# Optimization experiments

Hardware: AMD Instinct MI355X
Metric: run time of the kernel (lower is better)

## Reference

```python
import jax, jax.numpy as jnp
import numpy as np

N_HEAD = 12

def setup_inputs() -> dict:
    key = jax.random.key(0)
    k1, k2, k3, k4, k5 = jax.random.split(key, 5)
    B, T, C = 16, 1024, 768
    s = 0.02
    return {
        "x": jax.random.normal(k1, (B, T, C), dtype=jnp.float32),
        "W_attn": jax.random.normal(k2, (C, 3 * C), dtype=jnp.float32) * s,
        "b_attn": jax.random.normal(k3, (3 * C,), dtype=jnp.float32) * s,
        "W_proj": jax.random.normal(k4, (C, C), dtype=jnp.float32) * s,
        "b_proj": jax.random.normal(k5, (C,), dtype=jnp.float32) * s,
    }

def reference(x, W_attn, b_attn, W_proj, b_proj):
    B, T, C = x.shape
    H = N_HEAD
    d = C // H
    qkv = x @ W_attn + b_attn                      # [B,T,3C]
    q, k, v = jnp.split(qkv, 3, axis=-1)
    # [B,H,T,d]
    q = q.reshape(B, T, H, d).transpose(0, 2, 1, 3)
    k = k.reshape(B, T, H, d).transpose(0, 2, 1, 3)
    v = v.reshape(B, T, H, d).transpose(0, 2, 1, 3)
    scale = 1.0 / jnp.sqrt(jnp.array(d, dtype=x.dtype))
    att = jnp.einsum('bhqd,bhkd->bhqk', q, k) * scale   # [B,H,T,T]
    causal = jnp.tril(jnp.ones((T, T), dtype=bool))
    att = jnp.where(causal[None, None], att, -jnp.inf)
    att = jax.nn.softmax(att, axis=-1)
    # dropout is identity in eval mode (p=0 for deterministic reference)
    y = jnp.einsum('bhqk,bhkd->bhqd', att, v)            # [B,H,T,d]
    y = y.transpose(0, 2, 1, 3).reshape(B, T, C)
    return y @ W_proj + b_proj
```

## Files before the change

### kernel.cpp

```cpp
#include <hip/hip_runtime.h>
#include <cstddef>


typedef __bf16 bf16_t;
typedef __bf16 bf16x4 __attribute__((ext_vector_type(4)));
typedef __bf16 bf16x8 __attribute__((ext_vector_type(8)));
typedef float  f32x4  __attribute__((ext_vector_type(4)));

#define MFMA16(a,b,c) __builtin_amdgcn_mfma_f32_16x16x32_bf16((a),(b),(c),0,0,0)
#define GLOAD16(gp, lp) \
  __builtin_amdgcn_global_load_lds((const __attribute__((address_space(1))) unsigned int*)(gp), \
                                   (__attribute__((address_space(3))) unsigned int*)(lp), 16, 0, 0)

#define SWZ(row, c) (((row) * 64) + ((((c) ^ ((row) & 7)) * 8)))

#define QSCALE 0.1803368801111f

__global__ __launch_bounds__(256)
void xcast_kernel(const float* __restrict__ in, bf16_t* __restrict__ out)
{
    const size_t i = ((size_t)blockIdx.x * 256 + threadIdx.x) * 4;
    float4 f = *(const float4*)(in + i);
    bf16x4 o = {(bf16_t)f.x, (bf16_t)f.y, (bf16_t)f.z, (bf16_t)f.w};
    *(bf16x4*)(out + i) = o;
}

__global__ __launch_bounds__(256)
void tcast_kernel(const float* __restrict__ in, bf16_t* __restrict__ out, int R, int Cn)
{
    __shared__ bf16_t tile[32][33];
    const int tx = threadIdx.x & 31, ty = threadIdx.x >> 5;
    const int c0 = blockIdx.x * 32, r0 = blockIdx.y * 32;
#pragma unroll
    for (int i = 0; i < 4; ++i)
        tile[ty + i*8][tx] = (bf16_t)in[(size_t)(r0 + ty + i*8) * Cn + c0 + tx];
    __syncthreads();
#pragma unroll
    for (int i = 0; i < 4; ++i)
        out[(size_t)(c0 + ty + i*8) * R + r0 + tx] = tile[tx][ty + i*8];
}

__global__ __launch_bounds__(256)
void vtrans_kernel(const bf16_t* __restrict__ in, bf16_t* __restrict__ out)
{
    __shared__ bf16_t tile[32][33];
    const int tx = threadIdx.x & 31, ty = threadIdx.x >> 5;
    const int t0 = blockIdx.x * 32, c0 = blockIdx.y * 32;
    const size_t base = (size_t)blockIdx.z * 65536;
#pragma unroll
    for (int i = 0; i < 4; ++i)
        tile[ty + i*8][tx] = in[base + (size_t)(t0 + ty + i*8) * 64 + c0 + tx];
    __syncthreads();
#pragma unroll
    for (int i = 0; i < 4; ++i)
        out[base + (size_t)(c0 + ty + i*8) * 1024 + t0 + tx] = tile[tx][ty + i*8];
}

__global__ __launch_bounds__(256)
void qkv_gemm(const bf16_t* __restrict__ Xb, const bf16_t* __restrict__ WT,
              const float* __restrict__ bias,
              bf16_t* __restrict__ Qb, bf16_t* __restrict__ Kb, bf16_t* __restrict__ Vb)
{
    __shared__ bf16_t As[128 * 64];
    __shared__ bf16_t Bs[128 * 64];
    const int tid = threadIdx.x;
    const int w = tid >> 6, l = tid & 63;
    const int lm = l & 15, lq = l >> 4;
    const int wy = w >> 1, wx = w & 1;
    const int lr = l >> 3;
    const int lcs = ((l & 7) ^ lr) * 8;
    const int nt = blockIdx.x * 128, mt = blockIdx.y * 128;

    f32x4 acc[4][4];
    const f32x4 z4 = {0.f, 0.f, 0.f, 0.f};
#pragma unroll
    for (int i = 0; i < 4; ++i)
#pragma unroll
        for (int j = 0; j < 4; ++j) acc[i][j] = z4;

    for (int kt = 0; kt < 768; kt += 64) {
#pragma unroll
        for (int p = 0; p < 4; ++p) {
            const int row = w * 32 + p * 8;
            GLOAD16(Xb + (size_t)(mt + row + lr) * 768 + kt + lcs, &As[row * 64]);
            GLOAD16(WT + (size_t)(nt + row + lr) * 768 + kt + lcs, &Bs[row * 64]);
        }
        __syncthreads();
#pragma unroll
        for (int ks = 0; ks < 2; ++ks) {
            const int c = ks * 4 + lq;
            bf16x8 aw[4], bx[4];
#pragma unroll
            for (int i = 0; i < 4; ++i)
                aw[i] = *(const bf16x8*)(&Bs[SWZ(wx * 64 + i * 16 + lm, c)]);
#pragma unroll
            for (int j = 0; j < 4; ++j)
                bx[j] = *(const bf16x8*)(&As[SWZ(wy * 64 + j * 16 + lm, c)]);
#pragma unroll
            for (int i = 0; i < 4; ++i)
#pragma unroll
                for (int j = 0; j < 4; ++j)
                    acc[i][j] = MFMA16(aw[i], bx[j], acc[i][j]);
        }
        __syncthreads();
    }

    const int nb = nt + wx * 64;
    const int which = nb / 768;
    const int h = (nb % 768) >> 6;
    bf16_t* dst = (which == 0) ? Qb : ((which == 1) ? Kb : Vb);
    const float qs = (which == 0) ? QSCALE : 1.0f;
    const int b_ = mt >> 10;
    const int tbase = (mt & 1023) + wy * 64;
#pragma unroll
    for (int i = 0; i < 4; ++i) {
        const float4 bv = *(const float4*)(bias + nb + i * 16 + lq * 4);
        const int d0 = i * 16 + lq * 4;
#pragma unroll
        for (int j = 0; j < 4; ++j) {
            const int t = tbase + j * 16 + lm;
            f32x4 v = acc[i][j];
            bf16x4 o4 = {(bf16_t)((v[0] + bv.x) * qs), (bf16_t)((v[1] + bv.y) * qs),
                         (bf16_t)((v[2] + bv.z) * qs), (bf16_t)((v[3] + bv.w) * qs)};
            *(bf16x4*)(dst + ((size_t)(b_ * 12 + h) * 1024 + t) * 64 + d0) = o4;
        }
    }
}

__global__ __launch_bounds__(256, 3)
void attn_kernel(const bf16_t* __restrict__ Qb, const bf16_t* __restrict__ Kb,
                 const bf16_t* __restrict__ VT, bf16_t* __restrict__ Y)
{
    __shared__ bf16_t Ks[64 * 72];
    __shared__ bf16_t Vs[64 * 72];
    __shared__ bf16_t Plds[4 * 16 * 72];
    const int tid = threadIdx.x;
    const int w = tid >> 6, l = tid & 63;
    const int lm = l & 15, lq = l >> 4;
    const int r8 = tid >> 3, c8 = (tid & 7) * 8;
    const int xp = blockIdx.x;
    const int bh = blockIdx.y;
    const int loq = xp * 128, hiq = (7 - xp) * 128;

    int qmin[4];
    qmin[0] = loq + w * 32;      qmin[1] = qmin[0] + 16;
    qmin[2] = hiq + w * 32;      qmin[3] = qmin[2] + 16;

    const bf16_t* Kbase = Kb + (size_t)bh * 65536;
    const bf16_t* Vbase = VT + (size_t)bh * 65536;
    bf16_t* Pw = &Plds[w * 1152];

    bf16x8 bq[4][2];
#pragma unroll
    for (int m = 0; m < 4; ++m) {
        const bf16_t* Qp = Qb + ((size_t)bh * 1024 + qmin[m] + lm) * 64;
        bq[m][0] = *(const bf16x8*)(Qp + lq * 8);
        bq[m][1] = *(const bf16x8*)(Qp + 32 + lq * 8);
    }

    f32x4 O[4][4];
    float li[4] = {0.f, 0.f, 0.f, 0.f};
    const f32x4 z4 = {0.f, 0.f, 0.f, 0.f};
#pragma unroll
    for (int m = 0; m < 4; ++m)
#pragma unroll
        for (int s = 0; s < 4; ++s) O[m][s] = z4;

    const int kend = hiq + 64;
    bf16x8 kr0 = *(const bf16x8*)(Kbase + (size_t)r8 * 64 + c8);
    bf16x8 kr1 = *(const bf16x8*)(Kbase + (size_t)(32 + r8) * 64 + c8);
    bf16x8 vr0 = *(const bf16x8*)(Vbase + (size_t)r8 * 1024 + c8);
    bf16x8 vr1 = *(const bf16x8*)(Vbase + (size_t)(32 + r8) * 1024 + c8);

    for (int k0 = 0; k0 <= kend; k0 += 64) {
        if (k0) __syncthreads();
        *(bf16x8*)(&Ks[r8 * 72 + c8]) = kr0;
        *(bf16x8*)(&Ks[(32 + r8) * 72 + c8]) = kr1;
        *(bf16x8*)(&Vs[r8 * 72 + c8]) = vr0;
        *(bf16x8*)(&Vs[(32 + r8) * 72 + c8]) = vr1;
        __syncthreads();
        if (k0 + 64 <= kend) {
            kr0 = *(const bf16x8*)(Kbase + (size_t)(k0 + 64 + r8) * 64 + c8);
            kr1 = *(const bf16x8*)(Kbase + (size_t)(k0 + 96 + r8) * 64 + c8);
            vr0 = *(const bf16x8*)(Vbase + (size_t)r8 * 1024 + k0 + 64 + c8);
            vr1 = *(const bf16x8*)(Vbase + (size_t)(32 + r8) * 1024 + k0 + 64 + c8);
        }
#pragma unroll
        for (int m = 0; m < 4; ++m) {
            if (k0 > qmin[m] + 15) continue;
            f32x4 S[4];
#pragma unroll
            for (int s = 0; s < 4; ++s) S[s] = z4;
#pragma unroll
            for (int ks = 0; ks < 2; ++ks)
#pragma unroll
                for (int s = 0; s < 4; ++s) {
                    bf16x8 ak = *(const bf16x8*)(&Ks[(s * 16 + lm) * 72 + ks * 32 + lq * 8]);
                    S[s] = MFMA16(ak, bq[m][ks], S[s]);
                }
            if (k0 + 63 > qmin[m]) {
                const int q = qmin[m] + lm;
#pragma unroll
                for (int s = 0; s < 4; ++s)
#pragma unroll
                    for (int rg = 0; rg < 4; ++rg)
                        if (k0 + s * 16 + lq * 4 + rg > q) S[s][rg] = -1e30f;
            }
            float ls = 0.f;
#pragma unroll
            for (int s = 0; s < 4; ++s)
#pragma unroll
                for (int rg = 0; rg < 4; ++rg) {
                    float pv = exp2f(S[s][rg]);
                    S[s][rg] = pv;
                    ls += pv;
                }
            li[m] += ls;
#pragma unroll
            for (int s = 0; s < 4; ++s) {
                bf16x4 p4 = {(bf16_t)S[s][0], (bf16_t)S[s][1],
                             (bf16_t)S[s][2], (bf16_t)S[s][3]};
                *(bf16x4*)(&Pw[lm * 72 + s * 16 + lq * 4]) = p4;
            }
#pragma unroll
            for (int ks = 0; ks < 2; ++ks) {
                bf16x8 bp = *(const bf16x8*)(&Pw[lm * 72 + ks * 32 + lq * 8]);
#pragma unroll
                for (int s = 0; s < 4; ++s) {
                    bf16x8 av = *(const bf16x8*)(&Vs[(s * 16 + lm) * 72 + ks * 32 + lq * 8]);
                    O[m][s] = MFMA16(av, bp, O[m][s]);
                }
            }
        }
    }

    const int b = bh / 12, h = bh % 12;
#pragma unroll
    for (int m = 0; m < 4; ++m) {
        float s0 = li[m];
        s0 += __shfl_xor(s0, 16, 64);
        s0 += __shfl_xor(s0, 32, 64);
        const float inv = 1.f / s0;
        const size_t row = ((size_t)(b * 1024 + qmin[m] + lm)) * 768 + h * 64;
#pragma unroll
        for (int s = 0; s < 4; ++s) {
            bf16x4 y4 = {(bf16_t)(O[m][s][0] * inv), (bf16_t)(O[m][s][1] * inv),
                         (bf16_t)(O[m][s][2] * inv), (bf16_t)(O[m][s][3] * inv)};
            *(bf16x4*)(Y + row + s * 16 + lq * 4) = y4;
        }
    }
}

__global__ __launch_bounds__(256)
void proj_gemm(const bf16_t* __restrict__ A, const bf16_t* __restrict__ WT,
               const float* __restrict__ bias, float* __restrict__ out)
{
    __shared__ bf16_t As[128 * 64];
    __shared__ bf16_t Bs[128 * 64];
    const int tid = threadIdx.x;
    const int w = tid >> 6, l = tid & 63;
    const int lm = l & 15, lq = l >> 4;
    const int wy = w >> 1, wx = w & 1;
    const int lr = l >> 3;
    const int lcs = ((l & 7) ^ lr) * 8;
    const int nt = blockIdx.x * 128, mt = blockIdx.y * 128;

    f32x4 acc[4][4];
    const f32x4 z4 = {0.f, 0.f, 0.f, 0.f};
#pragma unroll
    for (int i = 0; i < 4; ++i)
#pragma unroll
        for (int j = 0; j < 4; ++j) acc[i][j] = z4;

    for (int kt = 0; kt < 768; kt += 64) {
#pragma unroll
        for (int p = 0; p < 4; ++p) {
            const int row = w * 32 + p * 8;
            GLOAD16(A  + (size_t)(mt + row + lr) * 768 + kt + lcs, &As[row * 64]);
            GLOAD16(WT + (size_t)(nt + row + lr) * 768 + kt + lcs, &Bs[row * 64]);
        }
        __syncthreads();
#pragma unroll
        for (int ks = 0; ks < 2; ++ks) {
            const int c = ks * 4 + lq;
            bf16x8 aw[4], bx[4];
#pragma unroll
            for (int i = 0; i < 4; ++i)
                aw[i] = *(const bf16x8*)(&Bs[SWZ(wx * 64 + i * 16 + lm, c)]);
#pragma unroll
            for (int j = 0; j < 4; ++j)
                bx[j] = *(const bf16x8*)(&As[SWZ(wy * 64 + j * 16 + lm, c)]);
#pragma unroll
            for (int i = 0; i < 4; ++i)
#pragma unroll
                for (int j = 0; j < 4; ++j)
                    acc[i][j] = MFMA16(aw[i], bx[j], acc[i][j]);
        }
        __syncthreads();
    }
#pragma unroll
    for (int i = 0; i < 4; ++i) {
        const int n0 = nt + wx * 64 + i * 16 + lq * 4;
        const float4 bv = *(const float4*)(bias + n0);
#pragma unroll
        for (int j = 0; j < 4; ++j) {
            const int t = mt + wy * 64 + j * 16 + lm;
            f32x4 v = acc[i][j];
            float4 o = {v[0] + bv.x, v[1] + bv.y, v[2] + bv.z, v[3] + bv.w};
            *(float4*)(out + (size_t)t * 768 + n0) = o;
        }
    }
}

extern "C" void kernel_launch(void* const* d_in, const int* in_sizes, int n_in,
                              void* d_out, int out_size, void* d_ws, size_t ws_size,
                              hipStream_t stream)
{
    const float* x      = (const float*)d_in[0];
    const float* W_attn = (const float*)d_in[1];
    const float* b_attn = (const float*)d_in[2];
    const float* W_proj = (const float*)d_in[3];
    const float* b_proj = (const float*)d_in[4];
    float* out = (float*)d_out;

    char* ws = (char*)d_ws;
    const size_t SZ = (size_t)16 * 12 * 1024 * 64 * 2;
    bf16_t* Qb  = (bf16_t*)(ws);
    bf16_t* Kb  = (bf16_t*)(ws + SZ);
    bf16_t* Vb  = (bf16_t*)(ws + 2 * SZ);
    bf16_t* VT  = (bf16_t*)(ws + 3 * SZ);
    bf16_t* Yb  = (bf16_t*)(ws + 4 * SZ);
    bf16_t* Xb  = (bf16_t*)(ws + 4 * SZ);
    bf16_t* WaT = (bf16_t*)(ws + 5 * SZ);
    bf16_t* WpT = (bf16_t*)(ws + 5 * SZ + (size_t)2304 * 768 * 2);

    xcast_kernel<<<12288, 256, 0, stream>>>(x, Xb);
    tcast_kernel<<<dim3(72, 24), 256, 0, stream>>>(W_attn, WaT, 768, 2304);
    tcast_kernel<<<dim3(24, 24), 256, 0, stream>>>(W_proj, WpT, 768, 768);
    qkv_gemm<<<dim3(18, 128), 256, 0, stream>>>(Xb, WaT, b_attn, Qb, Kb, Vb);
    vtrans_kernel<<<dim3(32, 2, 192), 256, 0, stream>>>(Vb, VT);
    attn_kernel<<<dim3(4, 192), 256, 0, stream>>>(Qb, Kb, VT, Yb);
    proj_gemm<<<dim3(6, 128), 256, 0, stream>>>(Yb, WpT, b_proj, out);
}
```

Baseline: 305.1 us.

## Fuse V transpose into QKV epilogue and double-buffer attention K/V via direct LDS loads

The QKV GEMM epilogue now writes V directly in transposed [d][t] layout, which removes the separate vtrans kernel and its extra round trip through global memory. The attention kernel replaces the register-staged K/V tile loads with global_load_lds into double-buffered, XOR-swizzled LDS tiles, so the next tile's loads overlap compute and each iteration needs one barrier instead of two. The transposed V writes are scalar 2-byte stores with strided addresses, which may coalesce poorly. LDS use in the attention kernel also grows, which could affect occupancy.

```diff
diff --git a/kernel.cpp b/kernel.cpp
--- a/kernel.cpp
+++ b/kernel.cpp
@@ -41,25 +41,9 @@
 }
 
 __global__ __launch_bounds__(256)
-void vtrans_kernel(const bf16_t* __restrict__ in, bf16_t* __restrict__ out)
-{
-    __shared__ bf16_t tile[32][33];
-    const int tx = threadIdx.x & 31, ty = threadIdx.x >> 5;
-    const int t0 = blockIdx.x * 32, c0 = blockIdx.y * 32;
-    const size_t base = (size_t)blockIdx.z * 65536;
-#pragma unroll
-    for (int i = 0; i < 4; ++i)
-        tile[ty + i*8][tx] = in[base + (size_t)(t0 + ty + i*8) * 64 + c0 + tx];
-    __syncthreads();
-#pragma unroll
-    for (int i = 0; i < 4; ++i)
-        out[base + (size_t)(c0 + ty + i*8) * 1024 + t0 + tx] = tile[tx][ty + i*8];
-}
-
-__global__ __launch_bounds__(256)
 void qkv_gemm(const bf16_t* __restrict__ Xb, const bf16_t* __restrict__ WT,
               const float* __restrict__ bias,
-              bf16_t* __restrict__ Qb, bf16_t* __restrict__ Kb, bf16_t* __restrict__ Vb)
+              bf16_t* __restrict__ Qb, bf16_t* __restrict__ Kb, bf16_t* __restrict__ VT)
 {
     __shared__ bf16_t As[128 * 64];
     __shared__ bf16_t Bs[128 * 64];
@@ -108,21 +92,39 @@
     const int nb = nt + wx * 64;
     const int which = nb / 768;
     const int h = (nb % 768) >> 6;
-    bf16_t* dst = (which == 0) ? Qb : ((which == 1) ? Kb : Vb);
-    const float qs = (which == 0) ? QSCALE : 1.0f;
     const int b_ = mt >> 10;
     const int tbase = (mt & 1023) + wy * 64;
-#pragma unroll
-    for (int i = 0; i < 4; ++i) {
-        const float4 bv = *(const float4*)(bias + nb + i * 16 + lq * 4);
-        const int d0 = i * 16 + lq * 4;
-#pragma unroll
-        for (int j = 0; j < 4; ++j) {
-            const int t = tbase + j * 16 + lm;
-            f32x4 v = acc[i][j];
-            bf16x4 o4 = {(bf16_t)((v[0] + bv.x) * qs), (bf16_t)((v[1] + bv.y) * qs),
-                         (bf16_t)((v[2] + bv.z) * qs), (bf16_t)((v[3] + bv.w) * qs)};
-            *(bf16x4*)(dst + ((size_t)(b_ * 12 + h) * 1024 + t) * 64 + d0) = o4;
+    if (which == 2) {
+        bf16_t* vt = VT + (size_t)(b_ * 12 + h) * 65536;
+#pragma unroll
+        for (int i = 0; i < 4; ++i) {
+            const float4 bv = *(const float4*)(bias + nb + i * 16 + lq * 4);
+            const int d0 = i * 16 + lq * 4;
+#pragma unroll
+            for (int j = 0; j < 4; ++j) {
+                const int t = tbase + j * 16 + lm;
+                f32x4 v = acc[i][j];
+                vt[(size_t)(d0 + 0) * 1024 + t] = (bf16_t)(v[0] + bv.x);
+                vt[(size_t)(d0 + 1) * 1024 + t] = (bf16_t)(v[1] + bv.y);
+                vt[(size_t)(d0 + 2) * 1024 + t] = (bf16_t)(v[2] + bv.z);
+                vt[(size_t)(d0 + 3) * 1024 + t] = (bf16_t)(v[3] + bv.w);
+            }
+        }
+    } else {
+        bf16_t* dst = (which == 0) ? Qb : Kb;
+        const float qs = (which == 0) ? QSCALE : 1.0f;
+#pragma unroll
+        for (int i = 0; i < 4; ++i) {
+            const float4 bv = *(const float4*)(bias + nb + i * 16 + lq * 4);
+            const int d0 = i * 16 + lq * 4;
+#pragma unroll
+            for (int j = 0; j < 4; ++j) {
+                const int t = tbase + j * 16 + lm;
+                f32x4 v = acc[i][j];
+                bf16x4 o4 = {(bf16_t)((v[0] + bv.x) * qs), (bf16_t)((v[1] + bv.y) * qs),
+                             (bf16_t)((v[2] + bv.z) * qs), (bf16_t)((v[3] + bv.w) * qs)};
+                *(bf16x4*)(dst + ((size_t)(b_ * 12 + h) * 1024 + t) * 64 + d0) = o4;
+            }
         }
     }
 }
@@ -131,13 +133,14 @@
 void attn_kernel(const bf16_t* __restrict__ Qb, const bf16_t* __restrict__ Kb,
                  const bf16_t* __restrict__ VT, bf16_t* __restrict__ Y)
 {
-    __shared__ bf16_t Ks[64 * 72];
-    __shared__ bf16_t Vs[64 * 72];
+    __shared__ bf16_t Ks[2][64 * 64];
+    __shared__ bf16_t Vs[2][64 * 64];
     __shared__ bf16_t Plds[4 * 16 * 72];
     const int tid = threadIdx.x;
     const int w = tid >> 6, l = tid & 63;
     const int lm = l & 15, lq = l >> 4;
-    const int r8 = tid >> 3, c8 = (tid & 7) * 8;
+    const int lr = l >> 3;
+    const int lc8 = ((l & 7) ^ lr) * 8;
     const int xp = blockIdx.x;
     const int bh = blockIdx.y;
     const int loq = xp * 128, hiq = (7 - xp) * 128;
@@ -149,6 +152,7 @@
     const bf16_t* Kbase = Kb + (size_t)bh * 65536;
     const bf16_t* Vbase = VT + (size_t)bh * 65536;
     bf16_t* Pw = &Plds[w * 1152];
+    const int r0a = w * 16, r0b = w * 16 + 8;
 
     bf16x8 bq[4][2];
 #pragma unroll
@@ -167,24 +171,32 @@
         for (int s = 0; s < 4; ++s) O[m][s] = z4;
 
     const int kend = hiq + 64;
-    bf16x8 kr0 = *(const bf16x8*)(Kbase + (size_t)r8 * 64 + c8);
-    bf16x8 kr1 = *(const bf16x8*)(Kbase + (size_t)(32 + r8) * 64 + c8);
-    bf16x8 vr0 = *(const bf16x8*)(Vbase + (size_t)r8 * 1024 + c8);
-    bf16x8 vr1 = *(const bf16x8*)(Vbase + (size_t)(32 + r8) * 1024 + c8);
-
+
+    GLOAD16(Kbase + (size_t)(r0a + lr) * 64 + lc8,   &Ks[0][r0a * 64]);
+    GLOAD16(Kbase + (size_t)(r0b + lr) * 64 + lc8,   &Ks[0][r0b * 64]);
+    GLOAD16(Vbase + (size_t)(r0a + lr) * 1024 + lc8, &Vs[0][r0a * 64]);
+    GLOAD16(Vbase + (size_t)(r0b + lr) * 1024 + lc8, &Vs[0][r0b * 64]);
+    __syncthreads();
+
+    int cb = 0;
     for (int k0 = 0; k0 <= kend; k0 += 64) {
-        if (k0) __syncthreads();
-        *(bf16x8*)(&Ks[r8 * 72 + c8]) = kr0;
-        *(bf16x8*)(&Ks[(32 + r8) * 72 + c8]) = kr1;
-        *(bf16x8*)(&Vs[r8 * 72 + c8]) = vr0;
-        *(bf16x8*)(&Vs[(32 + r8) * 72 + c8]) = vr1;
-        __syncthreads();
+        const int nxt = cb ^ 1;
         if (k0 + 64 <= kend) {
-            kr0 = *(const bf16x8*)(Kbase + (size_t)(k0 + 64 + r8) * 64 + c8);
-            kr1 = *(const bf16x8*)(Kbase + (size_t)(k0 + 96 + r8) * 64 + c8);
-            vr0 = *(const bf16x8*)(Vbase + (size_t)r8 * 1024 + k0 + 64 + c8);
-            vr1 = *(const bf16x8*)(Vbase + (size_t)(32 + r8) * 1024 + k0 + 64 + c8);
-        }
+            const int kn = k0 + 64;
+            if (nxt) {
+                GLOAD16(Kbase + (size_t)(kn + r0a + lr) * 64 + lc8,        &Ks[1][r0a * 64]);
+                GLOAD16(Kbase + (size_t)(kn + r0b + lr) * 64 + lc8,        &Ks[1][r0b * 64]);
+                GLOAD16(Vbase + (size_t)(r0a + lr) * 1024 + kn + lc8,      &Vs[1][r0a * 64]);
+                GLOAD16(Vbase + (size_t)(r0b + lr) * 1024 + kn + lc8,      &Vs[1][r0b * 64]);
+            } else {
+                GLOAD16(Kbase + (size_t)(kn + r0a + lr) * 64 + lc8,        &Ks[0][r0a * 64]);
+                GLOAD16(Kbase + (size_t)(kn + r0b + lr) * 64 + lc8,        &Ks[0][r0b * 64]);
+                GLOAD16(Vbase + (size_t)(r0a + lr) * 1024 + kn + lc8,      &Vs[0][r0a * 64]);
+                GLOAD16(Vbase + (size_t)(r0b + lr) * 1024 + kn + lc8,      &Vs[0][r0b * 64]);
+            }
+        }
+        const bf16_t* Kc = Ks[cb];
+        const bf16_t* Vc = Vs[cb];
 #pragma unroll
         for (int m = 0; m < 4; ++m) {
             if (k0 > qmin[m] + 15) continue;
@@ -195,7 +207,7 @@
             for (int ks = 0; ks < 2; ++ks)
 #pragma unroll
                 for (int s = 0; s < 4; ++s) {
-                    bf16x8 ak = *(const bf16x8*)(&Ks[(s * 16 + lm) * 72 + ks * 32 + lq * 8]);
+                    bf16x8 ak = *(const bf16x8*)(&Kc[SWZ(s * 16 + lm, ks * 4 + lq)]);
                     S[s] = MFMA16(ak, bq[m][ks], S[s]);
                 }
             if (k0 + 63 > qmin[m]) {
@@ -227,11 +239,13 @@
                 bf16x8 bp = *(const bf16x8*)(&Pw[lm * 72 + ks * 32 + lq * 8]);
 #pragma unroll
                 for (int s = 0; s < 4; ++s) {
-                    bf16x8 av = *(const bf16x8*)(&Vs[(s * 16 + lm) * 72 + ks * 32 + lq * 8]);
+                    bf16x8 av = *(const bf16x8*)(&Vc[SWZ(s * 16 + lm, ks * 4 + lq)]);
                     O[m][s] = MFMA16(av, bp, O[m][s]);
                 }
             }
         }
+        __syncthreads();
+        cb = nxt;
     }
 
     const int b = bh / 12, h = bh % 12;
@@ -327,7 +341,6 @@
     const size_t SZ = (size_t)16 * 12 * 1024 * 64 * 2;
     bf16_t* Qb  = (bf16_t*)(ws);
     bf16_t* Kb  = (bf16_t*)(ws + SZ);
-    bf16_t* Vb  = (bf16_t*)(ws + 2 * SZ);
     bf16_t* VT  = (bf16_t*)(ws + 3 * SZ);
     bf16_t* Yb  = (bf16_t*)(ws + 4 * SZ);
     bf16_t* Xb  = (bf16_t*)(ws + 4 * SZ);
@@ -337,8 +350,7 @@
     xcast_kernel<<<12288, 256, 0, stream>>>(x, Xb);
     tcast_kernel<<<dim3(72, 24), 256, 0, stream>>>(W_attn, WaT, 768, 2304);
     tcast_kernel<<<dim3(24, 24), 256, 0, stream>>>(W_proj, WpT, 768, 768);
-    qkv_gemm<<<dim3(18, 128), 256, 0, stream>>>(Xb, WaT, b_attn, Qb, Kb, Vb);
-    vtrans_kernel<<<dim3(32, 2, 192), 256, 0, stream>>>(Vb, VT);
+    qkv_gemm<<<dim3(18, 128), 256, 0, stream>>>(Xb, WaT, b_attn, Qb, Kb, VT);
     attn_kernel<<<dim3(4, 192), 256, 0, stream>>>(Qb, Kb, VT, Yb);
     proj_gemm<<<dim3(6, 128), 256, 0, stream>>>(Yb, WpT, b_proj, out);
 }
```

After: 296.6 us. -2.8%, faster.
